# Optimization experiments

Measured on AMD Instinct MI355X. Metric: run time of the kernel, lower is better.

The kernel has to match this reference:

```python
import jax, jax.numpy as jnp
import numpy as np
from jax import lax


def squash(s):
    # scale = |s|^2/(1+|s|^2); out = scale * s/|s| (eps-stabilized as in source)
    norm = jnp.sum(s * s, axis=-1, keepdims=True)
    return (norm / (1.0 + norm)) * (s / jnp.sqrt(norm + 1e-8))


def setup_inputs() -> dict:
    key = jax.random.key(0)
    k = jax.random.split(key, 4)
    B, H, C = 32, 64, 10
    x = jax.random.normal(k[0], (B, 3, H, H), jnp.float32)
    conv1_w = jax.random.normal(k[1], (256, 3, 9, 9), jnp.float32) * 0.06
    conv1_b = jnp.zeros((256,), jnp.float32)
    conv2_w = jax.random.normal(k[2], (256, 256, 9, 9), jnp.float32) * 0.02  # 256 = 8 caps * 32 routes
    conv2_b = jnp.zeros((256,), jnp.float32)
    route_w = jax.random.normal(k[3], (32, C, 8, 16), jnp.float32)  # [routes, classes, in_dim, out_dim]
    return {"x": x, "conv1_w": conv1_w, "conv1_b": conv1_b,
            "conv2_w": conv2_w, "conv2_b": conv2_b, "route_w": route_w}


def reference(x, conv1_w, conv1_b, conv2_w, conv2_b, route_w):
    dn = ("NCHW", "OIHW", "NCHW")
    # PrimaryCapsules: conv 3->256 k9 s1 + relu
    h = lax.conv_general_dilated(x, conv1_w, (1, 1), "VALID", dimension_numbers=dn)
    h = jax.nn.relu(h + conv1_b[None, :, None, None])
    # CapsuleLayer conv: 256 -> 8*32 k9 s2
    h = lax.conv_general_dilated(h, conv2_w, (2, 2), "VALID", dimension_numbers=dn)
    h = h + conv2_b[None, :, None, None]
    B, _, hh, ww = h.shape
    R, D = 32, 8  # num_routes, capsule dim
    # [B, R*D, h, w] -> [B, R, P, D], squash per capsule vector
    caps = h.reshape(B, R, D, hh, ww).transpose(0, 1, 3, 4, 2).reshape(B, R, hh * ww, D)
    caps = squash(caps)
    # DigitCapsules: per-route linear maps 8->16, shared over spatial positions
    u_hat = jnp.einsum("brpi,rcio->brpco", caps, route_w)  # [B, R, P, C, 16]
    C, O = u_hat.shape[3], u_hat.shape[4]
    u_hat = u_hat.reshape(B, R * hh * ww, C, O)  # [B, N, C, 16]
    b_log = jnp.zeros(u_hat.shape[:-1], u_hat.dtype)  # [B, N, C]
    num_routing = 3
    v = None
    for i in range(num_routing):
        c = jax.nn.softmax(b_log, axis=2)            # over classes (dim=2 in source)
        s = jnp.einsum("bnc,bnco->bco", c, u_hat)    # weighted sum over input caps
        v = squash(s)                                 # [B, C, 16]
        if i < num_routing - 1:
            b_log = b_log + jnp.einsum("bnco,bco->bnc", u_hat, v)  # agreement
    return v
```

## Files before the change

kernel.cpp:

```cpp
#include <hip/hip_runtime.h>
#include <hip/hip_bf16.h>
#include <stdint.h>

typedef __attribute__((ext_vector_type(8))) short short8;
typedef __attribute__((ext_vector_type(4))) float f32x4;
typedef unsigned int u32x4a __attribute__((vector_size(16)));
typedef unsigned int u32x4u __attribute__((vector_size(16), aligned(4)));

__device__ inline unsigned short f2bf(float f) {
    union { float f; uint32_t u; } v; v.f = f;
    uint32_t u = v.u;
    uint32_t r = (u + 0x7FFFu + ((u >> 16) & 1u)) >> 16;
    return (unsigned short)r;
}

__device__ inline void gl_lds16(const unsigned short* g, unsigned short* l) {
    __builtin_amdgcn_global_load_lds(
        (const uint32_t __attribute__((address_space(1)))*)(const void*)g,
        (uint32_t __attribute__((address_space(3)))*)(void*)l, 16, 0, 0);
}

__global__ void cvt_w1(const float* __restrict__ w, unsigned short* __restrict__ A1) {
    int idx = blockIdx.x * 256 + threadIdx.x;
    int row = idx >> 8, k = idx & 255;
    float v = (k < 243) ? w[row * 243 + k] : 0.f;
    A1[idx] = f2bf(v);
}

__global__ void cvt_w2(const float* __restrict__ w, unsigned short* __restrict__ A2t) {
    int idx = blockIdx.x * 256 + threadIdx.x;
    int j = idx & 7;
    int off16 = (idx >> 3) & 1023;
    int tile = idx >> 13;
    int tm = tile / 324, chunk = tile - tm * 324;
    int row = off16 >> 3, sw = off16 & 7;
    int koct = sw ^ (row & 7);
    int kk = chunk * 64 + koct * 8 + j;
    int oc = tm * 128 + row;
    int ic, ky, kx;
    if (kk < 18432) { ic = kk / 72; int rem = kk - ic * 72; ky = rem >> 3; kx = rem & 7; }
    else { int j2 = kk - 18432; ic = j2 / 9; ky = j2 - ic * 9; kx = 8; }
    A2t[idx] = f2bf(w[((oc * 256 + ic) * 9 + ky) * 9 + kx]);
}

__global__ __launch_bounds__(256) void conv1_gemm(
    const unsigned short* __restrict__ A,
    const float* __restrict__ x,
    const float* __restrict__ bias,
    unsigned short* __restrict__ h1)
{
    __shared__ __align__(16) unsigned short As[128 * 40];
    __shared__ __align__(16) unsigned short Bs[128 * 40];
    const int tid = threadIdx.x;
    const int m0 = blockIdx.y * 128;
    const int sx = (blockIdx.x & 7) * 98 + (blockIdx.x >> 3);
    const int n0 = sx * 128;
    const int lane = tid & 63;
    const int wave = tid >> 6;
    const int wy = wave & 1, wx = wave >> 1;
    const int l16 = lane & 15, q = lane >> 4;

    const int kp = tid & 15;
    const int gn = tid >> 4;
    int baseN[8];
#pragma unroll
    for (int j = 0; j < 8; ++j) {
        int n = n0 + gn * 8 + j;
        int b = n / 3136, p = n % 3136;
        int oy = p / 56, ox = p % 56;
        baseN[j] = b * 12288 + oy * 64 + ox;
    }

    f32x4 acc[4][4];
#pragma unroll
    for (int im = 0; im < 4; ++im)
#pragma unroll
        for (int in = 0; in < 4; ++in)
            acc[im][in] = (f32x4){0.f, 0.f, 0.f, 0.f};

    for (int k0 = 0; k0 < 256; k0 += 32) {
        __syncthreads();
#pragma unroll
        for (int s = 0; s < 2; ++s) {
            int slot = tid + s * 256;
            int row = slot >> 2, seg = slot & 3;
            u32x4a v = *(const u32x4a*)(A + (m0 + row) * 256 + k0 + seg * 8);
            *(u32x4a*)(&As[row * 40 + seg * 8]) = v;
        }
        int ka = k0 + 2 * kp, kb = ka + 1;
        int offa = 0, offb = 0;
        bool va = ka < 243, vb = kb < 243;
        if (va) { int c = ka / 81, t = ka % 81, ky = t / 9, kx = t % 9; offa = c * 4096 + ky * 64 + kx; }
        if (vb) { int c = kb / 81, t = kb % 81, ky = t / 9, kx = t % 9; offb = c * 4096 + ky * 64 + kx; }
#pragma unroll
        for (int j = 0; j < 8; ++j) {
            unsigned int ba = va ? (unsigned int)f2bf(x[baseN[j] + offa]) : 0u;
            unsigned int bb = vb ? (unsigned int)f2bf(x[baseN[j] + offb]) : 0u;
            *(unsigned int*)(&Bs[(gn * 8 + j) * 40 + 2 * kp]) = ba | (bb << 16);
        }
        __syncthreads();

        short8 af[4], bf[4];
#pragma unroll
        for (int im = 0; im < 4; ++im)
            af[im] = *(const short8*)(&As[(wy * 64 + im * 16 + l16) * 40 + q * 8]);
#pragma unroll
        for (int in = 0; in < 4; ++in)
            bf[in] = *(const short8*)(&Bs[(wx * 64 + in * 16 + l16) * 40 + q * 8]);
#pragma unroll
        for (int im = 0; im < 4; ++im)
#pragma unroll
            for (int in = 0; in < 4; ++in)
                acc[im][in] = __builtin_amdgcn_mfma_f32_16x16x32_bf16(af[im], bf[in], acc[im][in], 0, 0, 0);
    }

#pragma unroll
    for (int in = 0; in < 4; ++in) {
        int n = n0 + wx * 64 + in * 16 + l16;
        int b = n / 3136, p = n % 3136;
        int oy = p / 56, ox = p % 56;
#pragma unroll
        for (int im = 0; im < 4; ++im) {
#pragma unroll
            for (int r = 0; r < 4; ++r) {
                int oc = m0 + wy * 64 + im * 16 + q * 4 + r;
                float v = acc[im][in][r] + bias[oc];
                v = v > 0.f ? v : 0.f;
                h1[((b * 256 + oc) * 56 + oy) * 56 + ox] = f2bf(v);
            }
        }
    }
}

__global__ __launch_bounds__(256, 3) void conv2_gemm(
    const unsigned short* __restrict__ A2t,
    const unsigned short* __restrict__ h1,
    float* __restrict__ c2)
{
    __shared__ __align__(16) unsigned short As[2][8192];
    __shared__ __align__(16) unsigned short BsT[128 * 72];
    const int tid = threadIdx.x;
    const int sx = (blockIdx.x & 7) * 18 + (blockIdx.x >> 3);
    const int n0 = sx * 128;
    const int z = blockIdx.z;
    const int lane = tid & 63;
    const int wave = tid >> 6;
    const int wy = wave & 1, wx = wave >> 1;
    const int l16 = lane & 15, q = lane >> 4;

    int boff[4];
#pragma unroll
    for (int in = 0; in < 4; ++in) {
        int n = n0 + wx * 64 + in * 16 + l16;
        int b = n / 576, p = n % 576;
        int oy = p / 24, ox = p % 24;
        boff[in] = b * 802816 + (2 * oy) * 56 + 2 * ox;
    }
    const int tn = tid & 127, thalf = tid >> 7;
    int tbase;
    {
        int ng = n0 + tn;
        int b = ng / 576, p = ng % 576;
        int oy = p / 24, ox = p % 24;
        tbase = b * 802816 + (2 * oy) * 56 + 2 * ox + 8;
    }

    f32x4 acc[4][4];
#pragma unroll
    for (int im = 0; im < 4; ++im)
#pragma unroll
        for (int in = 0; in < 4; ++in)
            acc[im][in] = (f32x4){0.f, 0.f, 0.f, 0.f};

    const size_t tilebase = (size_t)blockIdx.y * 324 * 8192;

    auto issueA = [&](int c, int buf) {
        const unsigned short* at = A2t + tilebase + (size_t)c * 8192;
        int s0 = wave * 4;
#pragma unroll
        for (int i = 0; i < 4; ++i) {
            int sl = (s0 + i) * 64 + lane;
            gl_lds16(at + sl * 8, &As[buf][sl * 8]);
        }
    };
    auto loadBmain = [&](int c, short8 (&B)[2][4]) {
#pragma unroll
        for (int h = 0; h < 2; ++h) {
            int octk = c * 8 + h * 4 + q;
            int ic = octk / 9;
            int ky = octk - ic * 9;
            int off = ic * 3136 + ky * 56;
#pragma unroll
            for (int in = 0; in < 4; ++in) {
                u32x4u v = *(const u32x4u*)(h1 + boff[in] + off);
                B[h][in] = __builtin_bit_cast(short8, v);
            }
        }
    };
    auto computeChunk = [&](int buf, short8 (&B)[2][4]) {
#pragma unroll
        for (int h = 0; h < 2; ++h) {
            short8 af[4];
#pragma unroll
            for (int im = 0; im < 4; ++im) {
                int row = wy * 64 + im * 16 + l16;
                int koct = h * 4 + q;
                af[im] = *(const short8*)(&As[buf][(row * 8 + (koct ^ (row & 7))) * 8]);
            }
            __builtin_amdgcn_s_setprio(1);
#pragma unroll
            for (int im = 0; im < 4; ++im)
#pragma unroll
                for (int in = 0; in < 4; ++in)
                    acc[im][in] = __builtin_amdgcn_mfma_f32_16x16x32_bf16(
                        af[im], B[h][in], acc[im][in], 0, 0, 0);
            __builtin_amdgcn_s_setprio(0);
        }
    };

    short8 B0[2][4], B1[2][4];

    issueA(z, 0);
    loadBmain(z, B0);
    __asm__ volatile("s_waitcnt vmcnt(8)" ::: "memory");
    __builtin_amdgcn_s_barrier();
    __asm__ volatile("" ::: "memory");

    int c = z;
    for (int it = 0; it < 18; ++it) {
        issueA(c + 8, 1);
        loadBmain(c + 8, B1);
        __asm__ volatile("" ::: "memory");
        computeChunk(0, B0);
        __asm__ volatile("s_waitcnt vmcnt(8)" ::: "memory");
        __builtin_amdgcn_s_barrier();
        __asm__ volatile("" ::: "memory");

        if (it < 17) {
            issueA(c + 16, 0);
            loadBmain(c + 16, B0);
        } else {
            issueA(z + 288, 0);
        }
        __asm__ volatile("" ::: "memory");
        computeChunk(1, B1);
        __asm__ volatile("s_waitcnt vmcnt(8)" ::: "memory");
        __builtin_amdgcn_s_barrier();
        __asm__ volatile("" ::: "memory");
        c += 16;
    }

    int bt = 0;
    for (int ct = z + 288; ct < 324; ct += 8) {
        uint32_t bR[16];
        int base = ct * 64 + thalf * 32 - 18432;
#pragma unroll
        for (int p = 0; p < 16; ++p) {
            int j2 = base + 2 * p;
            int icA = j2 / 9, kyA = j2 - icA * 9;
            int icB = (j2 + 1) / 9, kyB = (j2 + 1) - icB * 9;
            uint32_t ba = h1[tbase + icA * 3136 + kyA * 56];
            uint32_t bb = h1[tbase + icB * 3136 + kyB * 56];
            bR[p] = ba | (bb << 16);
        }
        if (ct + 8 < 324) issueA(ct + 8, bt ^ 1);
        __syncthreads();
#pragma unroll
        for (int p = 0; p < 16; ++p)
            *(uint32_t*)(&BsT[tn * 72 + thalf * 32 + 2 * p]) = bR[p];
        __syncthreads();
#pragma unroll
        for (int h = 0; h < 2; ++h) {
            short8 af[4], bf[4];
#pragma unroll
            for (int im = 0; im < 4; ++im) {
                int row = wy * 64 + im * 16 + l16;
                int koct = h * 4 + q;
                af[im] = *(const short8*)(&As[bt][(row * 8 + (koct ^ (row & 7))) * 8]);
            }
#pragma unroll
            for (int in = 0; in < 4; ++in)
                bf[in] = *(const short8*)(&BsT[(wx * 64 + in * 16 + l16) * 72 + h * 32 + q * 8]);
#pragma unroll
            for (int im = 0; im < 4; ++im)
#pragma unroll
                for (int in = 0; in < 4; ++in)
                    acc[im][in] = __builtin_amdgcn_mfma_f32_16x16x32_bf16(
                        af[im], bf[in], acc[im][in], 0, 0, 0);
        }
        __syncthreads();
        bt ^= 1;
    }

    const int m0 = blockIdx.y * 128;
#pragma unroll
    for (int in = 0; in < 4; ++in) {
        int nn = n0 + wx * 64 + in * 16 + l16;
        int bb = nn / 576, pp = nn % 576;
#pragma unroll
        for (int im = 0; im < 4; ++im) {
#pragma unroll
            for (int r = 0; r < 4; ++r) {
                int oc = m0 + wy * 64 + im * 16 + q * 4 + r;
                atomicAdd(&c2[(bb * 256 + oc) * 576 + pp], acc[im][in][r]);
            }
        }
    }
}

__global__ void squash_caps(const float* __restrict__ c2, const float* __restrict__ bias,
                            float* __restrict__ caps) {
    int idx = blockIdx.x * 256 + threadIdx.x;
    int b = idx / 18432;
    int rp = idx % 18432;
    int r = rp / 576, p = rp % 576;
    float s[8]; float n2 = 0.f;
#pragma unroll
    for (int d = 0; d < 8; ++d) {
        s[d] = c2[(b * 256 + r * 8 + d) * 576 + p] + bias[r * 8 + d];
        n2 += s[d] * s[d];
    }
    float sc = (n2 / (1.f + n2)) / sqrtf(n2 + 1e-8f);
#pragma unroll
    for (int d = 0; d < 8; ++d)
        caps[idx * 8 + d] = sc * s[d];
}

__global__ __launch_bounds__(64) void capsum0(const float* __restrict__ caps,
                                              float* __restrict__ G) {
    int r = blockIdx.x, b = blockIdx.y;
    const float* cp = caps + (size_t)(b * 32 + r) * 4608;
    int tid = threadIdx.x;
    f32x4 s0 = (f32x4){0.f, 0.f, 0.f, 0.f}, s1 = s0;
    for (int jv = 0; jv < 9; ++jv) {
        const f32x4* qp = (const f32x4*)(cp + (jv * 64 + tid) * 8);
        s0 += qp[0]; s1 += qp[1];
    }
#pragma unroll
    for (int off = 32; off > 0; off >>= 1) {
#pragma unroll
        for (int k = 0; k < 4; ++k) {
            s0[k] += __shfl_down(s0[k], off, 64);
            s1[k] += __shfl_down(s1[k], off, 64);
        }
    }
    if (tid == 0) {
        float g[8] = {s0[0], s0[1], s0[2], s0[3], s1[0], s1[1], s1[2], s1[3]};
        float* gp = G + (size_t)((b * 32 + r) * 10) * 8;
        for (int cc = 0; cc < 10; ++cc)
#pragma unroll
            for (int ii = 0; ii < 8; ++ii) gp[cc * 8 + ii] = g[ii] * 0.1f;
    }
}

__global__ __launch_bounds__(64) void route_accum(const float* __restrict__ caps,
                                                  const float* __restrict__ W,
                                                  const float* __restrict__ V,
                                                  float* __restrict__ G) {
    int r = blockIdx.x, b = blockIdx.y;
    __shared__ float wv[80];
    __shared__ float red[80][64];
    int tid = threadIdx.x;
    for (int v = tid; v < 80; v += 64) {
        int cc = v >> 3, ii = v & 7;
        float s = 0.f;
#pragma unroll
        for (int o = 0; o < 16; ++o)
            s += W[((r * 10 + cc) * 8 + ii) * 16 + o] * V[(b * 10 + cc) * 16 + o];
        wv[v] = s;
    }
    __syncthreads();
    float g[80];
#pragma unroll
    for (int v = 0; v < 80; ++v) g[v] = 0.f;
    const float* cp = caps + (size_t)(b * 32 + r) * 4608;
    for (int j = 0; j < 9; ++j) {
        int p = j * 64 + tid;
        const f32x4* qp = (const f32x4*)(cp + p * 8);
        f32x4 c0 = qp[0], c1 = qp[1];
        float c8[8];
#pragma unroll
        for (int i = 0; i < 4; ++i) { c8[i] = c0[i]; c8[4 + i] = c1[i]; }
        float a[10]; float m = -1e30f;
#pragma unroll
        for (int cc = 0; cc < 10; ++cc) {
            float t = 0.f;
#pragma unroll
            for (int i = 0; i < 8; ++i) t += c8[i] * wv[cc * 8 + i];
            a[cc] = t; m = fmaxf(m, t);
        }
        float sum = 0.f;
#pragma unroll
        for (int cc = 0; cc < 10; ++cc) { a[cc] = __expf(a[cc] - m); sum += a[cc]; }
        float inv = 1.f / sum;
#pragma unroll
        for (int cc = 0; cc < 10; ++cc) {
            float w = a[cc] * inv;
#pragma unroll
            for (int i = 0; i < 8; ++i) g[cc * 8 + i] += w * c8[i];
        }
    }
#pragma unroll
    for (int v = 0; v < 80; ++v) red[v][tid] = g[v];
    __syncthreads();
    for (int v = tid; v < 80; v += 64) {
        float s = 0.f;
        for (int t = 0; t < 64; ++t) s += red[v][t];
        G[(b * 32 + r) * 80 + v] = s;
    }
}

__global__ __launch_bounds__(160) void sv_kernel(const float* __restrict__ G,
                                                 const float* __restrict__ W,
                                                 float* __restrict__ V,
                                                 float* __restrict__ out, int last) {
    int b = blockIdx.x;
    int c = threadIdx.x / 16, o = threadIdx.x % 16;
    __shared__ float sL[10][16];
    float s = 0.f;
    for (int r = 0; r < 32; ++r) {
        const float* g = G + ((b * 32 + r) * 10 + c) * 8;
        const float* w = W + ((r * 10 + c) * 8) * 16 + o;
#pragma unroll
        for (int i = 0; i < 8; ++i) s += g[i] * w[i * 16];
    }
    sL[c][o] = s;
    __syncthreads();
    float n2 = 0.f;
#pragma unroll
    for (int oo = 0; oo < 16; ++oo) { float t = sL[c][oo]; n2 += t * t; }
    float sc = (n2 / (1.f + n2)) / sqrtf(n2 + 1e-8f);
    float v = sc * s;
    V[(b * 10 + c) * 16 + o] += v;
    if (last) out[(b * 10 + c) * 16 + o] = v;
}

extern "C" void kernel_launch(void* const* d_in, const int* in_sizes, int n_in,
                              void* d_out, int out_size, void* d_ws, size_t ws_size,
                              hipStream_t stream) {
    const float* x  = (const float*)d_in[0];
    const float* w1 = (const float*)d_in[1];
    const float* b1 = (const float*)d_in[2];
    const float* w2 = (const float*)d_in[3];
    const float* b2 = (const float*)d_in[4];
    const float* rw = (const float*)d_in[5];

    char* ws = (char*)d_ws;
    unsigned short* A1   = (unsigned short*)(ws);
    unsigned short* A2   = (unsigned short*)(ws + 262144);
    unsigned short* h1   = (unsigned short*)(ws + 10878976);
    float*          c2   = (float*)(ws + 62259200);
    float*          caps = (float*)(ws + 81133568);
    float*          V    = (float*)(ws + 100007936);
    float*          G    = (float*)(ws + 100028416);

    hipLaunchKernelGGL(cvt_w1, dim3(256), dim3(256), 0, stream, w1, A1);
    hipLaunchKernelGGL(cvt_w2, dim3(20736), dim3(256), 0, stream, w2, A2);
    hipMemsetAsync(c2, 0, 18874368, stream);
    hipLaunchKernelGGL(conv1_gemm, dim3(784, 2), dim3(256), 0, stream, A1, x, b1, h1);
    hipLaunchKernelGGL(conv2_gemm, dim3(144, 2, 8), dim3(256), 0, stream, A2, h1, c2);
    hipLaunchKernelGGL(squash_caps, dim3(2304), dim3(256), 0, stream, c2, b2, caps);
    hipMemsetAsync(V, 0, 5120 * sizeof(float), stream);
    hipLaunchKernelGGL(capsum0, dim3(32, 32), dim3(64), 0, stream, caps, G);
    hipLaunchKernelGGL(sv_kernel, dim3(32), dim3(160), 0, stream, G, rw, V, (float*)d_out, 0);
    for (int it = 1; it < 3; ++it) {
        hipLaunchKernelGGL(route_accum, dim3(32, 32), dim3(64), 0, stream, caps, rw, V, G);
        hipLaunchKernelGGL(sv_kernel, dim3(32), dim3(160), 0, stream, G, rw, V,
                           (float*)d_out, it == 2 ? 1 : 0);
    }
}
```

Measured before the change: 457.1 us.

## Switch conv2 GEMM to 32x32x16 MFMA with new LDS swizzle

Replaces the 16x16x32 bf16 MFMA tiling in the conv2 implicit GEMM with 32x32x16 MFMA, so each wave computes a 2x2 grid of 32x32 tiles instead of 4x4 16x16 tiles. This cuts the number of A/B fragment loads per FLOP and the instruction count. The LDS swizzle and the weight pre-layout are changed to a new XOR pattern to avoid bank conflicts with the new access pattern. The tail B tile gets the same swizzled layout, replacing its padded layout, and the epilogue mapping is updated. Risks are a different register footprint and a different global access pattern for the B fragments.

```diff
diff --git a/kernel.cpp b/kernel.cpp
--- a/kernel.cpp
+++ b/kernel.cpp
@@ -4,6 +4,7 @@
 
 typedef __attribute__((ext_vector_type(8))) short short8;
 typedef __attribute__((ext_vector_type(4))) float f32x4;
+typedef __attribute__((ext_vector_type(16))) float f32x16;
 typedef unsigned int u32x4a __attribute__((vector_size(16)));
 typedef unsigned int u32x4u __attribute__((vector_size(16), aligned(4)));
 
@@ -19,6 +20,8 @@
         (const uint32_t __attribute__((address_space(1)))*)(const void*)g,
         (uint32_t __attribute__((address_space(3)))*)(void*)l, 16, 0, 0);
 }
+
+__device__ __host__ inline int swz(int row) { return (row & 7) ^ ((row >> 2) & 6); }
 
 __global__ void cvt_w1(const float* __restrict__ w, unsigned short* __restrict__ A1) {
     int idx = blockIdx.x * 256 + threadIdx.x;
@@ -34,7 +37,7 @@
     int tile = idx >> 13;
     int tm = tile / 324, chunk = tile - tm * 324;
     int row = off16 >> 3, sw = off16 & 7;
-    int koct = sw ^ (row & 7);
+    int koct = sw ^ swz(row);
     int kk = chunk * 64 + koct * 8 + j;
     int oc = tm * 128 + row;
     int ic, ky, kx;
@@ -138,7 +141,7 @@
     float* __restrict__ c2)
 {
     __shared__ __align__(16) unsigned short As[2][8192];
-    __shared__ __align__(16) unsigned short BsT[128 * 72];
+    __shared__ __align__(16) unsigned short BsT[8192];
     const int tid = threadIdx.x;
     const int sx = (blockIdx.x & 7) * 18 + (blockIdx.x >> 3);
     const int n0 = sx * 128;
@@ -146,16 +149,110 @@
     const int lane = tid & 63;
     const int wave = tid >> 6;
     const int wy = wave & 1, wx = wave >> 1;
-    const int l16 = lane & 15, q = lane >> 4;
-
-    int boff[4];
-#pragma unroll
-    for (int in = 0; in < 4; ++in) {
-        int n = n0 + wx * 64 + in * 16 + l16;
+    const int l32 = lane & 31, kh = lane >> 5;
+
+    int boff[2];
+#pragma unroll
+    for (int in = 0; in < 2; ++in) {
+        int n = n0 + wx * 64 + in * 32 + l32;
         int b = n / 576, p = n % 576;
         int oy = p / 24, ox = p % 24;
         boff[in] = b * 802816 + (2 * oy) * 56 + 2 * ox;
     }
+    int aoff[4][2];
+#pragma unroll
+    for (int s = 0; s < 4; ++s)
+#pragma unroll
+        for (int im = 0; im < 2; ++im) {
+            int row = wy * 64 + im * 32 + l32;
+            aoff[s][im] = (row * 8 + ((2 * s + kh) ^ swz(row))) * 8;
+        }
+
+    f32x16 acc[2][2];
+#pragma unroll
+    for (int im = 0; im < 2; ++im)
+#pragma unroll
+        for (int in = 0; in < 2; ++in)
+#pragma unroll
+            for (int r = 0; r < 16; ++r)
+                acc[im][in][r] = 0.f;
+
+    const size_t tilebase = (size_t)blockIdx.y * 324 * 8192;
+    const int s0 = wave * 4;
+
+    auto issueA = [&](int c, int buf) {
+        const unsigned short* at = A2t + tilebase + (size_t)c * 8192;
+#pragma unroll
+        for (int i = 0; i < 4; ++i) {
+            int sl = (s0 + i) * 64 + lane;
+            gl_lds16(at + sl * 8, &As[buf][sl * 8]);
+        }
+    };
+    auto loadB = [&](int c, short8 (&B)[4][2]) {
+#pragma unroll
+        for (int s = 0; s < 4; ++s) {
+            int octk = c * 8 + 2 * s + kh;
+            int ic = octk / 9;
+            int ky = octk - ic * 9;
+            int off = ic * 3136 + ky * 56;
+#pragma unroll
+            for (int in = 0; in < 2; ++in) {
+                u32x4u v = *(const u32x4u*)(h1 + boff[in] + off);
+                B[s][in] = __builtin_bit_cast(short8, v);
+            }
+        }
+    };
+    auto computeChunk = [&](int buf, short8 (&B)[4][2]) {
+        const unsigned short* ab = &As[buf][0];
+#pragma unroll
+        for (int s = 0; s < 4; ++s) {
+            short8 af[2];
+#pragma unroll
+            for (int im = 0; im < 2; ++im)
+                af[im] = *(const short8*)(ab + aoff[s][im]);
+            __builtin_amdgcn_s_setprio(1);
+#pragma unroll
+            for (int im = 0; im < 2; ++im)
+#pragma unroll
+                for (int in = 0; in < 2; ++in)
+                    acc[im][in] = __builtin_amdgcn_mfma_f32_32x32x16_bf16(
+                        af[im], B[s][in], acc[im][in], 0, 0, 0);
+            __builtin_amdgcn_s_setprio(0);
+        }
+    };
+
+    short8 B0[4][2], B1[4][2];
+
+    issueA(z, 0);
+    loadB(z, B0);
+    __asm__ volatile("s_waitcnt vmcnt(8)" ::: "memory");
+    __builtin_amdgcn_s_barrier();
+    __asm__ volatile("" ::: "memory");
+
+    int c = z;
+    for (int it = 0; it < 18; ++it) {
+        issueA(c + 8, 1);
+        loadB(c + 8, B1);
+        __asm__ volatile("" ::: "memory");
+        computeChunk(0, B0);
+        __asm__ volatile("s_waitcnt vmcnt(8)" ::: "memory");
+        __builtin_amdgcn_s_barrier();
+        __asm__ volatile("" ::: "memory");
+
+        if (it < 17) {
+            issueA(c + 16, 0);
+            loadB(c + 16, B0);
+        } else {
+            issueA(z + 288, 0);
+        }
+        __asm__ volatile("" ::: "memory");
+        computeChunk(1, B1);
+        __asm__ volatile("s_waitcnt vmcnt(8)" ::: "memory");
+        __builtin_amdgcn_s_barrier();
+        __asm__ volatile("" ::: "memory");
+        c += 16;
+    }
+
     const int tn = tid & 127, thalf = tid >> 7;
     int tbase;
     {
@@ -164,91 +261,14 @@
         int oy = p / 24, ox = p % 24;
         tbase = b * 802816 + (2 * oy) * 56 + 2 * ox + 8;
     }
-
-    f32x4 acc[4][4];
-#pragma unroll
-    for (int im = 0; im < 4; ++im)
-#pragma unroll
-        for (int in = 0; in < 4; ++in)
-            acc[im][in] = (f32x4){0.f, 0.f, 0.f, 0.f};
-
-    const size_t tilebase = (size_t)blockIdx.y * 324 * 8192;
-
-    auto issueA = [&](int c, int buf) {
-        const unsigned short* at = A2t + tilebase + (size_t)c * 8192;
-        int s0 = wave * 4;
-#pragma unroll
-        for (int i = 0; i < 4; ++i) {
-            int sl = (s0 + i) * 64 + lane;
-            gl_lds16(at + sl * 8, &As[buf][sl * 8]);
-        }
-    };
-    auto loadBmain = [&](int c, short8 (&B)[2][4]) {
-#pragma unroll
-        for (int h = 0; h < 2; ++h) {
-            int octk = c * 8 + h * 4 + q;
-            int ic = octk / 9;
-            int ky = octk - ic * 9;
-            int off = ic * 3136 + ky * 56;
-#pragma unroll
-            for (int in = 0; in < 4; ++in) {
-                u32x4u v = *(const u32x4u*)(h1 + boff[in] + off);
-                B[h][in] = __builtin_bit_cast(short8, v);
-            }
-        }
-    };
-    auto computeChunk = [&](int buf, short8 (&B)[2][4]) {
-#pragma unroll
-        for (int h = 0; h < 2; ++h) {
-            short8 af[4];
-#pragma unroll
-            for (int im = 0; im < 4; ++im) {
-                int row = wy * 64 + im * 16 + l16;
-                int koct = h * 4 + q;
-                af[im] = *(const short8*)(&As[buf][(row * 8 + (koct ^ (row & 7))) * 8]);
-            }
-            __builtin_amdgcn_s_setprio(1);
-#pragma unroll
-            for (int im = 0; im < 4; ++im)
-#pragma unroll
-                for (int in = 0; in < 4; ++in)
-                    acc[im][in] = __builtin_amdgcn_mfma_f32_16x16x32_bf16(
-                        af[im], B[h][in], acc[im][in], 0, 0, 0);
-            __builtin_amdgcn_s_setprio(0);
-        }
-    };
-
-    short8 B0[2][4], B1[2][4];
-
-    issueA(z, 0);
-    loadBmain(z, B0);
-    __asm__ volatile("s_waitcnt vmcnt(8)" ::: "memory");
-    __builtin_amdgcn_s_barrier();
-    __asm__ volatile("" ::: "memory");
-
-    int c = z;
-    for (int it = 0; it < 18; ++it) {
-        issueA(c + 8, 1);
-        loadBmain(c + 8, B1);
-        __asm__ volatile("" ::: "memory");
-        computeChunk(0, B0);
-        __asm__ volatile("s_waitcnt vmcnt(8)" ::: "memory");
-        __builtin_amdgcn_s_barrier();
-        __asm__ volatile("" ::: "memory");
-
-        if (it < 17) {
-            issueA(c + 16, 0);
-            loadBmain(c + 16, B0);
-        } else {
-            issueA(z + 288, 0);
-        }
-        __asm__ volatile("" ::: "memory");
-        computeChunk(1, B1);
-        __asm__ volatile("s_waitcnt vmcnt(8)" ::: "memory");
-        __builtin_amdgcn_s_barrier();
-        __asm__ volatile("" ::: "memory");
-        c += 16;
-    }
+    int boffT[4][2];
+#pragma unroll
+    for (int s = 0; s < 4; ++s)
+#pragma unroll
+        for (int in = 0; in < 2; ++in) {
+            int row = wx * 64 + in * 32 + l32;
+            boffT[s][in] = (row * 8 + ((2 * s + kh) ^ swz(row))) * 8;
+        }
 
     int bt = 0;
     for (int ct = z + 288; ct < 324; ct += 8) {
@@ -265,27 +285,30 @@
         }
         if (ct + 8 < 324) issueA(ct + 8, bt ^ 1);
         __syncthreads();
-#pragma unroll
-        for (int p = 0; p < 16; ++p)
-            *(uint32_t*)(&BsT[tn * 72 + thalf * 32 + 2 * p]) = bR[p];
+        {
+            int rsw = tn * 8, rx = swz(tn);
+#pragma unroll
+            for (int p = 0; p < 16; ++p) {
+                int col = thalf * 32 + 2 * p;
+                int a16 = (rsw + ((col >> 3) ^ rx)) * 8 + (col & 7);
+                *(uint32_t*)(&BsT[a16]) = bR[p];
+            }
+        }
         __syncthreads();
 #pragma unroll
-        for (int h = 0; h < 2; ++h) {
-            short8 af[4], bf[4];
-#pragma unroll
-            for (int im = 0; im < 4; ++im) {
-                int row = wy * 64 + im * 16 + l16;
-                int koct = h * 4 + q;
-                af[im] = *(const short8*)(&As[bt][(row * 8 + (koct ^ (row & 7))) * 8]);
-            }
-#pragma unroll
-            for (int in = 0; in < 4; ++in)
-                bf[in] = *(const short8*)(&BsT[(wx * 64 + in * 16 + l16) * 72 + h * 32 + q * 8]);
-#pragma unroll
-            for (int im = 0; im < 4; ++im)
-#pragma unroll
-                for (int in = 0; in < 4; ++in)
-                    acc[im][in] = __builtin_amdgcn_mfma_f32_16x16x32_bf16(
+        for (int s = 0; s < 4; ++s) {
+            short8 af[2], bf[2];
+#pragma unroll
+            for (int im = 0; im < 2; ++im)
+                af[im] = *(const short8*)(&As[bt][aoff[s][im]]);
+#pragma unroll
+            for (int in = 0; in < 2; ++in)
+                bf[in] = *(const short8*)(&BsT[boffT[s][in]]);
+#pragma unroll
+            for (int im = 0; im < 2; ++im)
+#pragma unroll
+                for (int in = 0; in < 2; ++in)
+                    acc[im][in] = __builtin_amdgcn_mfma_f32_32x32x16_bf16(
                         af[im], bf[in], acc[im][in], 0, 0, 0);
         }
         __syncthreads();
@@ -294,14 +317,15 @@
 
     const int m0 = blockIdx.y * 128;
 #pragma unroll
-    for (int in = 0; in < 4; ++in) {
-        int nn = n0 + wx * 64 + in * 16 + l16;
+    for (int in = 0; in < 2; ++in) {
+        int nn = n0 + wx * 64 + in * 32 + l32;
         int bb = nn / 576, pp = nn % 576;
 #pragma unroll
-        for (int im = 0; im < 4; ++im) {
-#pragma unroll
-            for (int r = 0; r < 4; ++r) {
-                int oc = m0 + wy * 64 + im * 16 + q * 4 + r;
+        for (int im = 0; im < 2; ++im) {
+#pragma unroll
+            for (int r = 0; r < 16; ++r) {
+                int crow = (r & 3) + 8 * (r >> 2) + 4 * kh;
+                int oc = m0 + wy * 64 + im * 32 + crow;
                 atomicAdd(&c2[(bb * 256 + oc) * 576 + pp], acc[im][in][r]);
             }
         }
```

New measurement: 493.8 us. +8.0%, slower.
